# Optimization experiments

Measured on AMD Instinct MI355X. Metric: run time of the kernel, lower is better.

The kernel has to match this reference:

```python
import jax, jax.numpy as jnp
import numpy as np

H = 256          # hidden_channels
R = 64           # num_rbf
N = 20000        # nodes
E = 320000       # edges
CUTOFF_LO = 0.0
CUTOFF_UP = 5.0
LN_EPS = 1e-5


def _layernorm(x, g, b):
    mu = jnp.mean(x, axis=-1, keepdims=True)
    var = jnp.var(x, axis=-1, keepdims=True)
    return (x - mu) * jax.lax.rsqrt(var + LN_EPS) * g + b


def _cosine_cutoff(r):
    # cutoff_lower == 0 branch of CosineCutoff
    c = 0.5 * (jnp.cos(r * (jnp.pi / CUTOFF_UP)) + 1.0)
    return c * (r < CUTOFF_UP).astype(r.dtype)


def setup_inputs() -> dict:
    key = jax.random.key(0)
    ks = jax.random.split(key, 16)
    def xavier(k, shape):
        fan_in, fan_out = shape[1], shape[0]
        lim = np.sqrt(6.0 / (fan_in + fan_out))
        return jax.random.uniform(k, shape, jnp.float32, -lim, lim)
    x = jax.random.normal(ks[0], (N, H), jnp.float32)
    edge_index = jax.random.randint(ks[1], (2, E), 0, N, jnp.int64)
    edge_weight = jax.random.uniform(ks[2], (E,), jnp.float32, 0.0, CUTOFF_UP)
    edge_attr = jax.random.normal(ks[3], (E, R), jnp.float32)
    return {
        "x": x,
        "edge_index": edge_index,
        "edge_weight": edge_weight,
        "edge_attr": edge_attr,
        "ln_g": jnp.ones((H,), jnp.float32),
        "ln_b": jnp.zeros((H,), jnp.float32),
        "Wq": xavier(ks[4], (H, H)), "bq": jnp.zeros((H,), jnp.float32),
        "Wk": xavier(ks[5], (H, H)), "bk": jnp.zeros((H,), jnp.float32),
        "Wv": xavier(ks[6], (H, H)), "bv": jnp.zeros((H,), jnp.float32),
        "Wo": xavier(ks[7], (H, H)), "bo": jnp.zeros((H,), jnp.float32),
        "Wdk": xavier(ks[8], (H, R)), "bdk": jnp.zeros((H,), jnp.float32),
        "Wdv": xavier(ks[9], (H, R)), "bdv": jnp.zeros((H,), jnp.float32),
    }


def reference(x, edge_index, edge_weight, edge_attr,
              ln_g, ln_b, Wq, bq, Wk, bk, Wv, bv, Wo, bo, Wdk, bdk, Wdv, bdv):
    src = edge_index[0]  # j (messages come from)
    dst = edge_index[1]  # i (messages aggregate to)

    x_norm = _layernorm(x, ln_g, ln_b)                     # [N,H]
    q = x_norm @ Wq.T + bq                                 # [N,H]
    k = x_norm @ Wk.T + bk
    v = x_norm @ Wv.T + bv

    dk = jax.nn.silu(edge_attr @ Wdk.T + bdk)              # [E,H]
    dv = jax.nn.silu(edge_attr @ Wdv.T + bdv)              # [E,H]

    q_i = q[dst]                                           # [E,H]
    k_j = k[src]
    v_j = v[src]

    attn = jnp.sum(q_i * k_j * dk, axis=1)                 # [E]
    attn = jax.nn.silu(attn) * _cosine_cutoff(edge_weight) # [E]

    msg = v_j * dv * attn[:, None]                         # [E,H]
    agg = jax.ops.segment_sum(msg, dst, num_segments=x.shape[0])  # [N,H]

    out = agg @ Wo.T + bo
    return x + out
```

## Files before the change

### kernel.cpp

```cpp
#include <hip/hip_runtime.h>
#include <math.h>

#define NN 20000
#define H 256
#define R 64
#define EE 320000
#define LN_EPS 1e-5f
#define NB 79

using short8  = __attribute__((ext_vector_type(8))) short;
using ushort8 = __attribute__((ext_vector_type(8))) unsigned short;
using f32x4   = __attribute__((ext_vector_type(4))) float;

__device__ __forceinline__ float silu_f(float x) { return x / (1.0f + __expf(-x)); }

__device__ __forceinline__ unsigned short f2bf(float f) {
    unsigned u = __float_as_uint(f);
    u += 0x7fff + ((u >> 16) & 1);
    return (unsigned short)(u >> 16);
}
__device__ __forceinline__ float bf2f(unsigned short s) {
    return __uint_as_float(((unsigned)s) << 16);
}

__device__ __forceinline__ int sw_idx(int row, int col) {
    return row * 64 + ((((col >> 3) ^ (row & 7)) << 3) | (col & 7));
}
__device__ __forceinline__ int dk_idx(int row, int col) {
    return row * 128 + (col ^ (((row >> 2) & 1) << 4));
}

__global__ __launch_bounds__(256) void k_prep(
    const float* __restrict__ Wq, const float* __restrict__ Wk,
    const float* __restrict__ Wv, const float* __restrict__ Wo,
    const float* __restrict__ g,  const float* __restrict__ b,
    const float* __restrict__ bq, const float* __restrict__ bk, const float* __restrict__ bv,
    const float* __restrict__ Wdk, const float* __restrict__ Wdv,
    unsigned short* __restrict__ wqkv_p, unsigned short* __restrict__ wo_p,
    unsigned short* __restrict__ wdk_p,  unsigned short* __restrict__ wdv_p,
    float* __restrict__ bias3)
{
    const int bid = blockIdx.x, t = threadIdx.x;
    if (bid < 128) {
        const int mat = bid >> 5;
        const float* W = mat == 0 ? Wq : (mat == 1 ? Wk : (mat == 2 ? Wv : Wo));
        unsigned short* out = (mat < 3) ? wqkv_p + (size_t)mat * 131072 : wo_p;
        const int fold = mat < 3;
        const int flat = (bid & 31) * 256 + t;
        const int tile = flat >> 9;
        const int rem  = flat & 511;
        const int ks   = rem >> 6;
        const int lane = rem & 63;
        const int nl = lane & 15, quad = lane >> 4;
        const int h  = tile * 16 + nl;
        const int c0 = ks * 32 + quad * 8;
        short8 hi8, lo8;
        #pragma unroll
        for (int j = 0; j < 8; ++j) {
            float wv = W[(size_t)h * 256 + c0 + j];
            if (fold) wv *= g[c0 + j];
            const unsigned short hh = f2bf(wv);
            hi8[j] = (short)hh;
            lo8[j] = (short)f2bf(wv - bf2f(hh));
        }
        unsigned short* ob = out + ((size_t)(tile * 8 + ks)) * 1024;
        *(short8*)&ob[lane * 8] = hi8;
        *(short8*)&ob[512 + lane * 8] = lo8;
    } else if (bid < 160) {
        const int flat = (bid - 128) * 256 + t;
        const int mat  = flat >> 12;
        const int rem  = flat & 4095;
        const int hh   = rem >> 11;
        const int r2   = rem & 2047;
        const int row  = r2 >> 4;
        const int col4 = (r2 & 15) * 4;
        const float* W = mat == 0 ? Wdk : Wdv;
        unsigned short* out = (mat == 0 ? wdk_p : wdv_p) + hh * 16384;
        const float4 w4 = *(const float4*)(W + (size_t)(hh * 128 + row) * 64 + col4);
        const unsigned short h0 = f2bf(w4.x), h1 = f2bf(w4.y), h2 = f2bf(w4.z), h3 = f2bf(w4.w);
        ushort4 hi4 = {h0, h1, h2, h3};
        ushort4 lo4 = {f2bf(w4.x - bf2f(h0)), f2bf(w4.y - bf2f(h1)),
                       f2bf(w4.z - bf2f(h2)), f2bf(w4.w - bf2f(h3))};
        const int di = sw_idx(row, col4);
        *(ushort4*)&out[di] = hi4;
        *(ushort4*)&out[8192 + di] = lo4;
    } else {
        const int mat = bid - 160, h = t;
        const float* W  = mat == 0 ? Wq : (mat == 1 ? Wk : Wv);
        const float* bb = mat == 0 ? bq : (mat == 1 ? bk : bv);
        float s = 0.f;
        const float* wr = W + (size_t)h * 256;
        for (int c = 0; c < 256; c += 4) {
            const float4 w4 = *(const float4*)(wr + c);
            const float4 b4 = *(const float4*)(b + c);
            s += w4.x * b4.x + w4.y * b4.y + w4.z * b4.z + w4.w * b4.w;
        }
        bias3[mat * 256 + h] = bb[h] + s;
    }
}

__global__ __launch_bounds__(256, 2) void k_ln_qkv(
    const float* __restrict__ x,
    const unsigned short* __restrict__ wqkv_p, const float* __restrict__ bias3,
    float* __restrict__ q, float* __restrict__ k, float* __restrict__ v)
{
    const int t = threadIdx.x;
    const int lane = t & 63, wave = t >> 6;
    const int nl = lane & 15, quad = lane >> 4;
    const int nbase = blockIdx.x * 64 + wave * 16;
    const int node = nbase + nl;
    const bool nv = node < NN;

    float xv[64];
    float sum = 0.f, sq = 0.f;
    {
        const float* xp = x + (size_t)node * H + quad * 8;
        #pragma unroll
        for (int ks = 0; ks < 8; ++ks) {
            float4 x0 = {0.f,0.f,0.f,0.f}, x1 = {0.f,0.f,0.f,0.f};
            if (nv) {
                x0 = *(const float4*)(xp + ks * 32);
                x1 = *(const float4*)(xp + ks * 32 + 4);
            }
            xv[ks*8+0]=x0.x; xv[ks*8+1]=x0.y; xv[ks*8+2]=x0.z; xv[ks*8+3]=x0.w;
            xv[ks*8+4]=x1.x; xv[ks*8+5]=x1.y; xv[ks*8+6]=x1.z; xv[ks*8+7]=x1.w;
            sum += x0.x+x0.y+x0.z+x0.w + x1.x+x1.y+x1.z+x1.w;
            sq  += x0.x*x0.x+x0.y*x0.y+x0.z*x0.z+x0.w*x0.w
                 + x1.x*x1.x+x1.y*x1.y+x1.z*x1.z+x1.w*x1.w;
        }
    }
    sum += __shfl_xor(sum, 16); sum += __shfl_xor(sum, 32);
    sq  += __shfl_xor(sq, 16);  sq  += __shfl_xor(sq, 32);
    const float mu  = sum * (1.0f / H);
    const float var = sq * (1.0f / H) - mu * mu;
    const float rs  = rsqrtf(var + LN_EPS);

    short8 a_hi[8], a_lo[8];
    #pragma unroll
    for (int ks = 0; ks < 8; ++ks) {
        #pragma unroll
        for (int j = 0; j < 8; ++j) {
            const float z = (xv[ks*8+j] - mu) * rs;
            const unsigned short hh = f2bf(z);
            a_hi[ks][j] = (short)hh;
            a_lo[ks][j] = (short)f2bf(z - bf2f(hh));
        }
    }

    for (int mat = 0; mat < 3; ++mat) {
        float* outp = mat == 0 ? q : (mat == 1 ? k : v);
        const float* bp = bias3 + mat * 256;
        const unsigned short* wb = wqkv_p + (size_t)mat * 131072 + lane * 8;
        for (int tile = 0; tile < 16; ++tile) {
            const unsigned short* gb = wb + (size_t)tile * 8192;
            const float bbv = bp[tile * 16 + nl];
            f32x4 acc = {bbv, bbv, bbv, bbv};
            #pragma unroll
            for (int ks = 0; ks < 8; ++ks) {
                const short8 b_hi = *(const short8*)(gb + ks * 1024);
                const short8 b_lo = *(const short8*)(gb + ks * 1024 + 512);
                acc = __builtin_amdgcn_mfma_f32_16x16x32_bf16(a_hi[ks], b_hi, acc, 0, 0, 0);
                acc = __builtin_amdgcn_mfma_f32_16x16x32_bf16(a_lo[ks], b_hi, acc, 0, 0, 0);
                acc = __builtin_amdgcn_mfma_f32_16x16x32_bf16(a_hi[ks], b_lo, acc, 0, 0, 0);
            }
            #pragma unroll
            for (int r = 0; r < 4; ++r) {
                const int onode = nbase + quad * 4 + r;
                if (onode < NN)
                    outp[(size_t)onode * H + tile * 16 + nl] = acc[r];
            }
        }
    }
}

__global__ __launch_bounds__(256) void k_hist(const int* __restrict__ ei, int* __restrict__ hist) {
    int e = blockIdx.x * 256 + threadIdx.x;
    if (e < EE) atomicAdd(&hist[ei[EE + e]], 1);
}

__global__ __launch_bounds__(256) void k_scan1(const int* __restrict__ hist,
                                               int* __restrict__ cursor, int* __restrict__ bsum) {
    const int t = threadIdx.x, i = blockIdx.x * 256 + t;
    const int lane = t & 63, w = t >> 6;
    const int v = (i < NN) ? hist[i] : 0;
    int incl = v;
    #pragma unroll
    for (int off = 1; off < 64; off <<= 1) {
        int u = __shfl_up(incl, off);
        if (lane >= off) incl += u;
    }
    __shared__ int ws[4];
    if (lane == 63) ws[w] = incl;
    __syncthreads();
    int base = 0;
    #pragma unroll
    for (int j = 0; j < 4; ++j) if (j < w) base += ws[j];
    if (i < NN) cursor[i] = base + incl - v;
    if (t == 255) bsum[blockIdx.x] = base + incl;
}

__global__ __launch_bounds__(128) void k_scan2(int* __restrict__ bsum) {
    __shared__ int buf[128];
    const int t = threadIdx.x;
    const int v = (t < NB) ? bsum[t] : 0;
    buf[t] = v;
    __syncthreads();
    #pragma unroll
    for (int off = 1; off < 128; off <<= 1) {
        int add = (t >= off) ? buf[t - off] : 0;
        __syncthreads();
        buf[t] += add;
        __syncthreads();
    }
    if (t < NB) bsum[t] = buf[t] - v;
}

__global__ __launch_bounds__(256) void k_scan3(int* __restrict__ cursor, const int* __restrict__ bsum) {
    const int i = blockIdx.x * 256 + threadIdx.x;
    if (i < NN) cursor[i] += bsum[blockIdx.x];
}

__global__ __launch_bounds__(256) void k_scatter(const int* __restrict__ ei,
                                                 int* __restrict__ cursor, int* __restrict__ perm) {
    int e = blockIdx.x * 256 + threadIdx.x;
    if (e < EE) {
        int d = ei[EE + e];
        int pos = atomicAdd(&cursor[d], 1);
        perm[pos] = e;
    }
}

__global__ __launch_bounds__(256, 3) void k_edge(
    const float* __restrict__ q, const float* __restrict__ k, const float* __restrict__ v,
    const int* __restrict__ ei, const float* __restrict__ ew, const float* __restrict__ ea,
    const unsigned short* __restrict__ wdk_p, const float* __restrict__ bdk,
    const unsigned short* __restrict__ wdv_p, const float* __restrict__ bdv,
    const int* __restrict__ perm,
    float* __restrict__ agg)
{
    __shared__ unsigned short ea_hi_s[64 * 64], ea_lo_s[64 * 64];
    __shared__ unsigned short w_region[2 * 128 * 64];
    __shared__ float attn_s[64];
    __shared__ int src_s[64], dst_s[64];

    unsigned short* w_hi_s = w_region;
    unsigned short* w_lo_s = w_region + 128 * 64;
    float* dks = (float*)w_region;

    const int t    = threadIdx.x;
    const int bi   = blockIdx.x;
    const int eb   = ((bi & 7) * 625 + (bi >> 3)) * 64;
    const int lane = t & 63, wave = t >> 6;
    const int nl   = lane & 15, quad = lane >> 4;
    const int estrip = wave * 16;
    const int tx = t & 31, ty = t >> 5;
    const int h0 = tx * 4, e0 = ty * 8;

    if (t < 64) {
        const int e = perm[eb + t];
        src_s[t] = ei[e];
        dst_s[t] = ei[EE + e];
        attn_s[t] = 0.f;
    }
    {
        const int row = t >> 2, seg = t & 3;
        const int e = perm[eb + row];
        const float* sp = ea + (size_t)e * R + seg * 16;
        #pragma unroll
        for (int j = 0; j < 4; ++j) {
            const float4 x4 = *(const float4*)(sp + 4 * j);
            const int di = sw_idx(row, seg * 16 + 4 * j);
            const unsigned short a0 = f2bf(x4.x), a1 = f2bf(x4.y),
                                 a2 = f2bf(x4.z), a3 = f2bf(x4.w);
            ushort4 hi4 = {a0, a1, a2, a3};
            ushort4 lo4 = {f2bf(x4.x - bf2f(a0)), f2bf(x4.y - bf2f(a1)),
                           f2bf(x4.z - bf2f(a2)), f2bf(x4.w - bf2f(a3))};
            *(ushort4*)&ea_hi_s[di] = hi4;
            *(ushort4*)&ea_lo_s[di] = lo4;
        }
    }
    __syncthreads();

    short8 a_hi[2], a_lo[2];
    {
        const int arow = estrip + nl;
        #pragma unroll
        for (int ks = 0; ks < 2; ++ks) {
            const int idx = arow * 64 + ((((ks * 4 + quad) ^ (nl & 7)) << 3));
            a_hi[ks] = *(const short8*)&ea_hi_s[idx];
            a_lo[ks] = *(const short8*)&ea_lo_s[idx];
        }
    }

    for (int hh = 0; hh < 2; ++hh) {
        __syncthreads();
        {
            const ushort8* sp = (const ushort8*)(wdk_p + (size_t)hh * 16384) + t;
            ushort8* dp = (ushort8*)w_region + t;
            #pragma unroll
            for (int c = 0; c < 8; ++c) dp[c * 256] = sp[c * 256];
        }
        __syncthreads();

        f32x4 accA[8];
        #pragma unroll
        for (int tt = 0; tt < 8; ++tt) {
            const int wrow = tt * 16 + nl;
            const int hcol = hh * 128 + tt * 16 + nl;
            short8 b_hi[2], b_lo[2];
            #pragma unroll
            for (int ks = 0; ks < 2; ++ks) {
                const int idx = wrow * 64 + ((((ks * 4 + quad) ^ (nl & 7)) << 3));
                b_hi[ks] = *(const short8*)&w_hi_s[idx];
                b_lo[ks] = *(const short8*)&w_lo_s[idx];
            }
            const float bb = bdk[hcol];
            f32x4 acc = {bb, bb, bb, bb};
            #pragma unroll
            for (int ks = 0; ks < 2; ++ks) {
                acc = __builtin_amdgcn_mfma_f32_16x16x32_bf16(a_hi[ks], b_hi[ks], acc, 0, 0, 0);
                acc = __builtin_amdgcn_mfma_f32_16x16x32_bf16(a_lo[ks], b_hi[ks], acc, 0, 0, 0);
                acc = __builtin_amdgcn_mfma_f32_16x16x32_bf16(a_hi[ks], b_lo[ks], acc, 0, 0, 0);
            }
            accA[tt] = acc;
        }
        __syncthreads();
        #pragma unroll
        for (int tt = 0; tt < 8; ++tt)
            #pragma unroll
            for (int r = 0; r < 4; ++r)
                dks[dk_idx(estrip + quad * 4 + r, tt * 16 + nl)] = silu_f(accA[tt][r]);
        __syncthreads();

        #pragma unroll
        for (int i = 0; i < 8; ++i) {
            const int d = dst_s[e0 + i], s = src_s[e0 + i];
            const float4 qi  = *(const float4*)(q + (size_t)d * H + hh * 128 + h0);
            const float4 kj  = *(const float4*)(k + (size_t)s * H + hh * 128 + h0);
            const float4 dk4 = *(const float4*)&dks[dk_idx(e0 + i, h0)];
            float part = qi.x * kj.x * dk4.x + qi.y * kj.y * dk4.y
                       + qi.z * kj.z * dk4.z + qi.w * kj.w * dk4.w;
            #pragma unroll
            for (int off = 16; off; off >>= 1) part += __shfl_xor(part, off);
            if (tx == 0) attn_s[e0 + i] += part;
        }
    }
    __syncthreads();
    if (t < 64) {
        const int e = perm[eb + t];
        const float rr = ew[e];
        const float cut = (rr < 5.0f) ? 0.5f * (__cosf(rr * 0.6283185307f) + 1.0f) : 0.0f;
        attn_s[t] = silu_f(attn_s[t]) * cut;
    }

    for (int hh = 0; hh < 2; ++hh) {
        __syncthreads();
        {
            const ushort8* sp = (const ushort8*)(wdv_p + (size_t)hh * 16384) + t;
            ushort8* dp = (ushort8*)w_region + t;
            #pragma unroll
            for (int c = 0; c < 8; ++c) dp[c * 256] = sp[c * 256];
        }
        __syncthreads();

        f32x4 accA[8];
        #pragma unroll
        for (int tt = 0; tt < 8; ++tt) {
            const int wrow = tt * 16 + nl;
            const int hcol = hh * 128 + tt * 16 + nl;
            short8 b_hi[2], b_lo[2];
            #pragma unroll
            for (int ks = 0; ks < 2; ++ks) {
                const int idx = wrow * 64 + ((((ks * 4 + quad) ^ (nl & 7)) << 3));
                b_hi[ks] = *(const short8*)&w_hi_s[idx];
                b_lo[ks] = *(const short8*)&w_lo_s[idx];
            }
            const float bb = bdv[hcol];
            f32x4 acc = {bb, bb, bb, bb};
            #pragma unroll
            for (int ks = 0; ks < 2; ++ks) {
                acc = __builtin_amdgcn_mfma_f32_16x16x32_bf16(a_hi[ks], b_hi[ks], acc, 0, 0, 0);
                acc = __builtin_amdgcn_mfma_f32_16x16x32_bf16(a_lo[ks], b_hi[ks], acc, 0, 0, 0);
                acc = __builtin_amdgcn_mfma_f32_16x16x32_bf16(a_hi[ks], b_lo[ks], acc, 0, 0, 0);
            }
            accA[tt] = acc;
        }
        __syncthreads();
        #pragma unroll
        for (int tt = 0; tt < 8; ++tt)
            #pragma unroll
            for (int r = 0; r < 4; ++r)
                dks[dk_idx(estrip + quad * 4 + r, tt * 16 + nl)] = silu_f(accA[tt][r]);
        __syncthreads();

        float4 m = {0.f, 0.f, 0.f, 0.f};
        int cur_d = -1;
        #pragma unroll
        for (int i = 0; i < 8; ++i) {
            const int d = dst_s[e0 + i], s = src_s[e0 + i];
            const float a = attn_s[e0 + i];
            const float4 vj  = *(const float4*)(v + (size_t)s * H + hh * 128 + h0);
            const float4 dv4 = *(const float4*)&dks[dk_idx(e0 + i, h0)];
            float4 mi;
            mi.x = vj.x * dv4.x * a;
            mi.y = vj.y * dv4.y * a;
            mi.z = vj.z * dv4.z * a;
            mi.w = vj.w * dv4.w * a;
            if (d != cur_d) {
                if (cur_d >= 0) {
                    float* dp = agg + (size_t)cur_d * H + hh * 128 + h0;
                    atomicAdd(dp + 0, m.x); atomicAdd(dp + 1, m.y);
                    atomicAdd(dp + 2, m.z); atomicAdd(dp + 3, m.w);
                }
                m = mi; cur_d = d;
            } else {
                m.x += mi.x; m.y += mi.y; m.z += mi.z; m.w += mi.w;
            }
        }
        {
            float* dp = agg + (size_t)cur_d * H + hh * 128 + h0;
            atomicAdd(dp + 0, m.x); atomicAdd(dp + 1, m.y);
            atomicAdd(dp + 2, m.z); atomicAdd(dp + 3, m.w);
        }
    }
}

__global__ __launch_bounds__(256, 2) void k_out(
    const float* __restrict__ aggm, const unsigned short* __restrict__ wo_p,
    const float* __restrict__ bo, const float* __restrict__ x, float* __restrict__ out)
{
    const int t = threadIdx.x;
    const int lane = t & 63, wave = t >> 6;
    const int nl = lane & 15, quad = lane >> 4;
    const int nbase = blockIdx.x * 64 + wave * 16;
    const int node = nbase + nl;
    const bool nv = node < NN;

    short8 a_hi[8], a_lo[8];
    {
        const float* ap = aggm + (size_t)node * H + quad * 8;
        #pragma unroll
        for (int ks = 0; ks < 8; ++ks) {
            float4 x0 = {0.f,0.f,0.f,0.f}, x1 = {0.f,0.f,0.f,0.f};
            if (nv) { x0 = *(const float4*)(ap + ks * 32); x1 = *(const float4*)(ap + ks * 32 + 4); }
            const float zz[8] = {x0.x,x0.y,x0.z,x0.w,x1.x,x1.y,x1.z,x1.w};
            #pragma unroll
            for (int j = 0; j < 8; ++j) {
                const unsigned short hh = f2bf(zz[j]);
                a_hi[ks][j] = (short)hh;
                a_lo[ks][j] = (short)f2bf(zz[j] - bf2f(hh));
            }
        }
    }
    for (int tile = 0; tile < 16; ++tile) {
        const unsigned short* gb = wo_p + (size_t)tile * 8192 + lane * 8;
        const float bbv = bo[tile * 16 + nl];
        f32x4 acc = {bbv, bbv, bbv, bbv};
        #pragma unroll
        for (int ks = 0; ks < 8; ++ks) {
            const short8 b_hi = *(const short8*)(gb + ks * 1024);
            const short8 b_lo = *(const short8*)(gb + ks * 1024 + 512);
            acc = __builtin_amdgcn_mfma_f32_16x16x32_bf16(a_hi[ks], b_hi, acc, 0, 0, 0);
            acc = __builtin_amdgcn_mfma_f32_16x16x32_bf16(a_lo[ks], b_hi, acc, 0, 0, 0);
            acc = __builtin_amdgcn_mfma_f32_16x16x32_bf16(a_hi[ks], b_lo, acc, 0, 0, 0);
        }
        #pragma unroll
        for (int r = 0; r < 4; ++r) {
            const int onode = nbase + quad * 4 + r;
            if (onode < NN) {
                const size_t oi = (size_t)onode * H + tile * 16 + nl;
                out[oi] = x[oi] + acc[r];
            }
        }
    }
}

extern "C" void kernel_launch(void* const* d_in, const int* in_sizes, int n_in,
                              void* d_out, int out_size, void* d_ws, size_t ws_size,
                              hipStream_t stream) {
    const float* x   = (const float*)d_in[0];
    const int*   ei  = (const int*)d_in[1];
    const float* ew  = (const float*)d_in[2];
    const float* ea  = (const float*)d_in[3];
    const float* g   = (const float*)d_in[4];
    const float* b   = (const float*)d_in[5];
    const float* Wq  = (const float*)d_in[6];  const float* bq  = (const float*)d_in[7];
    const float* Wk  = (const float*)d_in[8];  const float* bk  = (const float*)d_in[9];
    const float* Wv  = (const float*)d_in[10]; const float* bv  = (const float*)d_in[11];
    const float* Wo  = (const float*)d_in[12]; const float* bo  = (const float*)d_in[13];
    const float* Wdk = (const float*)d_in[14]; const float* bdk = (const float*)d_in[15];
    const float* Wdv = (const float*)d_in[16]; const float* bdv = (const float*)d_in[17];

    float* q    = (float*)d_ws;
    float* k    = q + (size_t)NN * H;
    float* v    = k + (size_t)NN * H;
    float* agg  = v + (size_t)NN * H;
    int*   hist = (int*)(agg + (size_t)NN * H);
    int*   cur  = hist + NN;
    int*   bsum = cur + NN;
    int*   perm = bsum + 128;
    unsigned short* wqkv_p = (unsigned short*)(perm + EE);
    unsigned short* wo_p   = wqkv_p + 393216;
    unsigned short* wdk_p  = wo_p + 131072;
    unsigned short* wdv_p  = wdk_p + 32768;
    float* bias3 = (float*)(wdv_p + 32768);

    hipMemsetAsync(hist, 0, NN * sizeof(int), stream);
    hipMemsetAsync(agg, 0, (size_t)NN * H * sizeof(float), stream);
    k_prep<<<163, 256, 0, stream>>>(Wq, Wk, Wv, Wo, g, b, bq, bk, bv, Wdk, Wdv,
                                    wqkv_p, wo_p, wdk_p, wdv_p, bias3);
    k_hist<<<EE / 256, 256, 0, stream>>>(ei, hist);
    k_ln_qkv<<<(NN + 63) / 64, 256, 0, stream>>>(x, wqkv_p, bias3, q, k, v);
    k_scan1<<<NB, 256, 0, stream>>>(hist, cur, bsum);
    k_scan2<<<1, 128, 0, stream>>>(bsum);
    k_scan3<<<NB, 256, 0, stream>>>(cur, bsum);
    k_scatter<<<EE / 256, 256, 0, stream>>>(ei, cur, perm);
    k_edge<<<EE / 64, 256, 0, stream>>>(q, k, v, ei, ew, ea, wdk_p, bdk, wdv_p, bdv, perm, agg);
    k_out<<<(NN + 63) / 64, 256, 0, stream>>>(agg, wo_p, bo, x, (float*)d_out);
}
```

Before: 647.3 us.

## Load edge_attr directly into registers, use global_load_lds for weights, shrink node blocks

The edge kernel no longer stages edge_attr through LDS. Each lane loads its own row from global memory and splits it into bf16 hi/lo in registers, which removes two LDS arrays and a barrier. Weight tiles are now copied with direct global-to-LDS loads instead of going through registers. The smaller LDS footprint lets the edge kernel raise its occupancy target to 4 blocks, and the LN/QKV and output kernels switch to single-wave 64-thread blocks with four times as many blocks. The risks are less coalesced edge_attr reads, more register pressure at higher occupancy, and correctness depending on the wave-uniform LDS base that global_load_lds expects.

```diff
diff --git a/kernel.cpp b/kernel.cpp
--- a/kernel.cpp
+++ b/kernel.cpp
@@ -11,6 +11,9 @@
 using short8  = __attribute__((ext_vector_type(8))) short;
 using ushort8 = __attribute__((ext_vector_type(8))) unsigned short;
 using f32x4   = __attribute__((ext_vector_type(4))) float;
+
+typedef __attribute__((address_space(3))) unsigned int lds_uint;
+typedef const __attribute__((address_space(1))) unsigned int glb_uint;
 
 __device__ __forceinline__ float silu_f(float x) { return x / (1.0f + __expf(-x)); }
 
@@ -99,15 +102,15 @@
     }
 }
 
-__global__ __launch_bounds__(256, 2) void k_ln_qkv(
+__global__ __launch_bounds__(64, 2) void k_ln_qkv(
     const float* __restrict__ x,
     const unsigned short* __restrict__ wqkv_p, const float* __restrict__ bias3,
     float* __restrict__ q, float* __restrict__ k, float* __restrict__ v)
 {
     const int t = threadIdx.x;
-    const int lane = t & 63, wave = t >> 6;
+    const int lane = t & 63;
     const int nl = lane & 15, quad = lane >> 4;
-    const int nbase = blockIdx.x * 64 + wave * 16;
+    const int nbase = blockIdx.x * 16;
     const int node = nbase + nl;
     const bool nv = node < NN;
 
@@ -230,7 +233,7 @@
     }
 }
 
-__global__ __launch_bounds__(256, 3) void k_edge(
+__global__ __launch_bounds__(256, 4) void k_edge(
     const float* __restrict__ q, const float* __restrict__ k, const float* __restrict__ v,
     const int* __restrict__ ei, const float* __restrict__ ew, const float* __restrict__ ea,
     const unsigned short* __restrict__ wdk_p, const float* __restrict__ bdk,
@@ -238,8 +241,7 @@
     const int* __restrict__ perm,
     float* __restrict__ agg)
 {
-    __shared__ unsigned short ea_hi_s[64 * 64], ea_lo_s[64 * 64];
-    __shared__ unsigned short w_region[2 * 128 * 64];
+    __shared__ __align__(16) unsigned short w_region[2 * 128 * 64];
     __shared__ float attn_s[64];
     __shared__ int src_s[64], dst_s[64];
 
@@ -262,33 +264,22 @@
         dst_s[t] = ei[EE + e];
         attn_s[t] = 0.f;
     }
-    {
-        const int row = t >> 2, seg = t & 3;
-        const int e = perm[eb + row];
-        const float* sp = ea + (size_t)e * R + seg * 16;
-        #pragma unroll
-        for (int j = 0; j < 4; ++j) {
-            const float4 x4 = *(const float4*)(sp + 4 * j);
-            const int di = sw_idx(row, seg * 16 + 4 * j);
-            const unsigned short a0 = f2bf(x4.x), a1 = f2bf(x4.y),
-                                 a2 = f2bf(x4.z), a3 = f2bf(x4.w);
-            ushort4 hi4 = {a0, a1, a2, a3};
-            ushort4 lo4 = {f2bf(x4.x - bf2f(a0)), f2bf(x4.y - bf2f(a1)),
-                           f2bf(x4.z - bf2f(a2)), f2bf(x4.w - bf2f(a3))};
-            *(ushort4*)&ea_hi_s[di] = hi4;
-            *(ushort4*)&ea_lo_s[di] = lo4;
-        }
-    }
-    __syncthreads();
 
     short8 a_hi[2], a_lo[2];
     {
-        const int arow = estrip + nl;
+        const int e = perm[eb + estrip + nl];
+        const float* ap = ea + (size_t)e * R + quad * 8;
         #pragma unroll
         for (int ks = 0; ks < 2; ++ks) {
-            const int idx = arow * 64 + ((((ks * 4 + quad) ^ (nl & 7)) << 3));
-            a_hi[ks] = *(const short8*)&ea_hi_s[idx];
-            a_lo[ks] = *(const short8*)&ea_lo_s[idx];
+            const float4 x0 = *(const float4*)(ap + ks * 32);
+            const float4 x1 = *(const float4*)(ap + ks * 32 + 4);
+            const float zz[8] = {x0.x, x0.y, x0.z, x0.w, x1.x, x1.y, x1.z, x1.w};
+            #pragma unroll
+            for (int j = 0; j < 8; ++j) {
+                const unsigned short hv = f2bf(zz[j]);
+                a_hi[ks][j] = (short)hv;
+                a_lo[ks][j] = (short)f2bf(zz[j] - bf2f(hv));
+            }
         }
     }
 
@@ -296,9 +287,11 @@
         __syncthreads();
         {
             const ushort8* sp = (const ushort8*)(wdk_p + (size_t)hh * 16384) + t;
-            ushort8* dp = (ushort8*)w_region + t;
-            #pragma unroll
-            for (int c = 0; c < 8; ++c) dp[c * 256] = sp[c * 256];
+            ushort8* dpw = (ushort8*)w_region + (t & 192);
+            #pragma unroll
+            for (int c = 0; c < 8; ++c)
+                __builtin_amdgcn_global_load_lds((glb_uint*)(sp + c * 256),
+                                                 (lds_uint*)(dpw + c * 256), 16, 0, 0);
         }
         __syncthreads();
 
@@ -357,9 +350,11 @@
         __syncthreads();
         {
             const ushort8* sp = (const ushort8*)(wdv_p + (size_t)hh * 16384) + t;
-            ushort8* dp = (ushort8*)w_region + t;
-            #pragma unroll
-            for (int c = 0; c < 8; ++c) dp[c * 256] = sp[c * 256];
+            ushort8* dpw = (ushort8*)w_region + (t & 192);
+            #pragma unroll
+            for (int c = 0; c < 8; ++c)
+                __builtin_amdgcn_global_load_lds((glb_uint*)(sp + c * 256),
+                                                 (lds_uint*)(dpw + c * 256), 16, 0, 0);
         }
         __syncthreads();
 
@@ -425,14 +420,14 @@
     }
 }
 
-__global__ __launch_bounds__(256, 2) void k_out(
+__global__ __launch_bounds__(64, 2) void k_out(
     const float* __restrict__ aggm, const unsigned short* __restrict__ wo_p,
     const float* __restrict__ bo, const float* __restrict__ x, float* __restrict__ out)
 {
     const int t = threadIdx.x;
-    const int lane = t & 63, wave = t >> 6;
+    const int lane = t & 63;
     const int nl = lane & 15, quad = lane >> 4;
-    const int nbase = blockIdx.x * 64 + wave * 16;
+    const int nbase = blockIdx.x * 16;
     const int node = nbase + nl;
     const bool nv = node < NN;
 
@@ -510,11 +505,11 @@
     k_prep<<<163, 256, 0, stream>>>(Wq, Wk, Wv, Wo, g, b, bq, bk, bv, Wdk, Wdv,
                                     wqkv_p, wo_p, wdk_p, wdv_p, bias3);
     k_hist<<<EE / 256, 256, 0, stream>>>(ei, hist);
-    k_ln_qkv<<<(NN + 63) / 64, 256, 0, stream>>>(x, wqkv_p, bias3, q, k, v);
+    k_ln_qkv<<<(NN + 15) / 16, 64, 0, stream>>>(x, wqkv_p, bias3, q, k, v);
     k_scan1<<<NB, 256, 0, stream>>>(hist, cur, bsum);
     k_scan2<<<1, 128, 0, stream>>>(bsum);
     k_scan3<<<NB, 256, 0, stream>>>(cur, bsum);
     k_scatter<<<EE / 256, 256, 0, stream>>>(ei, cur, perm);
     k_edge<<<EE / 64, 256, 0, stream>>>(q, k, v, ei, ew, ea, wdk_p, bdk, wdv_p, bdv, perm, agg);
-    k_out<<<(NN + 63) / 64, 256, 0, stream>>>(agg, wo_p, bo, x, (float*)d_out);
-}
+    k_out<<<(NN + 15) / 16, 64, 0, stream>>>(agg, wo_p, bo, x, (float*)d_out);
+}
```

After: 651.3 us. About the same (+0.6%).
